# Performance work log

Measured on AMD Instinct MI355X. Metric: run time of the kernel, lower is better.

The kernel has to match this reference:

```python
import jax, jax.numpy as jnp
import numpy as np

H, DQK, DV, DM, POS = 8, 64, 64, 768, 64

def _rel_basis(l, n):
    # Enformer central-mask relative position basis: [l, l, n]
    pos = jnp.arange(l)
    distance = pos[None, :] - pos[:, None]              # [l, l] int
    half = n // 2
    pow_rate = jnp.exp(jnp.log(jnp.asarray((l + 1) / 2.0, jnp.float32)) / half)
    center_widths = pow_rate ** jnp.arange(1, half + 1, dtype=jnp.float32)  # [half]
    unsigned = (jnp.abs(distance)[:, :, None].astype(jnp.float32) <= center_widths)
    signed = jnp.sign(distance)[:, :, None] * unsigned
    return jnp.concatenate([unsigned.astype(jnp.float32), signed.astype(jnp.float32)], axis=-1)

def setup_inputs() -> dict:
    key = jax.random.key(0)
    ks = jax.random.split(key, 9)
    b, l = 2, 1024
    x = jax.random.normal(ks[0], (b, l, DM), jnp.float32)
    # torch Linear weights: [out, in]
    Wq = jax.random.normal(ks[1], (H * DQK, DM), jnp.float32) * (1.0 / np.sqrt(DM))
    Wk = jax.random.normal(ks[2], (H * DQK, DM), jnp.float32) * (1.0 / np.sqrt(DM))
    Wv = jax.random.normal(ks[3], (H * DV, DM), jnp.float32) * (1.0 / np.sqrt(DM))
    Wo = jax.random.normal(ks[4], (DM, H * DV), jnp.float32) * (1.0 / np.sqrt(H * DV))
    bo = jnp.zeros((DM,), jnp.float32)
    u_bias = jax.random.normal(ks[5], (H, DQK), jnp.float32) * np.sqrt(2.0 / DQK)
    v_bias = jax.random.normal(ks[6], (H, DQK), jnp.float32) * np.sqrt(2.0 / DQK)
    w_pos = jax.random.normal(ks[7], (H, DQK, POS), jnp.float32) * np.sqrt(2.0 / POS)
    return {"x": x, "Wq": Wq, "Wk": Wk, "Wv": Wv, "Wo": Wo, "bo": bo,
            "u_bias": u_bias, "v_bias": v_bias, "w_pos": w_pos}

def reference(x, Wq, Wk, Wv, Wo, bo, u_bias, v_bias, w_pos):
    b, l, _ = x.shape
    q = (x @ Wq.T).reshape(b, l, H, DQK)
    k = (x @ Wk.T).reshape(b, l, H, DQK)
    v = (x @ Wv.T).reshape(b, l, H, DV)
    basis = _rel_basis(l, POS)                           # [l, l, n]
    scale = 1.0 / np.sqrt(DQK)
    # qr_term: einsum('bihd,hdn,ijn->bhij') factored to avoid [b,h,l,l,d]
    qw = jnp.einsum('bihd,hdn->bhin', q, w_pos)          # [b,h,l,n]
    qr = jnp.einsum('bhin,ijn->bhij', qw, basis)
    uk = jnp.einsum('hd,bjhd->bhj', u_bias, k)[:, :, None, :]
    vw = jnp.einsum('hd,hdn->hn', v_bias, w_pos)
    vr = jnp.einsum('hn,ijn->hij', vw, basis)[None]      # [1,h,l,l]
    bias = (qr + uk + vr) * scale
    scores = jnp.einsum('bihd,bjhd->bhij', q, k) * scale + bias
    attn = jax.nn.softmax(scores, axis=-1)
    out = jnp.einsum('bhij,bjhd->bihd', attn, v).reshape(b, l, H * DV)
    return out @ Wo.T + bo
```

## Files before the change

### kernel.cpp

```cpp
#include <hip/hip_runtime.h>

#define LSEQ 1024
#define NB   2
#define NH   8
#define DD   64
#define DMOD 768

using bf16x8 = __attribute__((ext_vector_type(8))) short;
using f32x4  = __attribute__((ext_vector_type(4))) float;

__device__ inline unsigned short f2bf(float f) {
    union { float f; unsigned u; } v; v.f = f;
    unsigned r = v.u + 0x7FFFu + ((v.u >> 16) & 1u);
    return (unsigned short)(r >> 16);
}

__global__ __launch_bounds__(256) void pack_setup(
    const float4* __restrict__ x,  const float4* __restrict__ wq,
    const float4* __restrict__ wk, const float4* __restrict__ wv,
    const float4* __restrict__ wo,
    const float* __restrict__ u_bias, const float* __restrict__ v_bias,
    const float* __restrict__ w_pos,
    ushort4* __restrict__ xb, ushort4* __restrict__ wqb, ushort4* __restrict__ wkb,
    ushort4* __restrict__ wvb, ushort4* __restrict__ wob,
    float* __restrict__ wsfx, unsigned char* __restrict__ cls_g)
{
    int tid = threadIdx.x;
    if (blockIdx.x >= 3072) {
        int sb = blockIdx.x - 3072;
        if (sb == 0) {
            __shared__ float w_s[32];
            __shared__ int cmin_s[1024];
            if (tid < 32) {
                float pr = expf(logf(512.5f) / 32.0f);
                w_s[tid] = powf(pr, (float)(tid + 1));
            }
            __syncthreads();
            for (int d = tid; d < 1024; d += 256) {
                float fd = (float)d;
                int cm = 32;
                for (int c = 31; c >= 0; --c) if (fd <= w_s[c]) cm = c;
                cmin_s[d] = cm;
            }
            __syncthreads();
            for (int d2 = tid; d2 < 2048; d2 += 256) {
                int dd = d2 - 1023;
                int ad = dd < 0 ? -dd : dd; if (ad > 1023) ad = 1023;
                int t = (dd < 0) ? 0 : ((dd == 0) ? 1 : 2);
                cls_g[d2] = (unsigned char)(t * 33 + cmin_s[ad]);
            }
        } else {
            int h = sb - 1;
            __shared__ float vred[4][64];
            __shared__ float ured[4][64];
            __shared__ float wd[64];
            int n = tid & 63, g = tid >> 6;
            float vs = 0.f, us = 0.f;
#pragma unroll
            for (int k = 0; k < 16; ++k) {
                int d = g * 16 + k;
                float wp = w_pos[(h * 64 + d) * 64 + n];
                vs += v_bias[h * 64 + d] * wp;
                us += u_bias[h * 64 + d] * wp;
            }
            vred[g][n] = vs; ured[g][n] = us;
            __syncthreads();
            if (tid < 64) {
                float v4 = vred[0][tid] + vred[1][tid] + vred[2][tid] + vred[3][tid];
                float u4 = ured[0][tid] + ured[1][tid] + ured[2][tid] + ured[3][tid];
                wd[tid] = v4 - u4;
            }
            __syncthreads();
            if (tid < 64) {
                int nn = tid & 31, cb = tid & 32;
                float s = 0.f;
                for (int c = 31; c >= nn; --c) s += wd[cb + c];
                wsfx[h * 64 + tid] = s * 0.125f;
            }
        }
        return;
    }
    int i = blockIdx.x * 256 + tid;
    const float4* src; ushort4* dst; int off;
    if (i < 393216)      { src = x;  dst = xb;  off = i; }
    else if (i < 491520) { src = wq; dst = wqb; off = i - 393216; }
    else if (i < 589824) { src = wk; dst = wkb; off = i - 491520; }
    else if (i < 688128) { src = wv; dst = wvb; off = i - 589824; }
    else                 { src = wo; dst = wob; off = i - 688128; }
    float4 v = src[off];
    ushort4 o;
    o.x = f2bf(v.x); o.y = f2bf(v.y); o.z = f2bf(v.z); o.w = f2bf(v.w);
    dst[off] = o;
}

__global__ __launch_bounds__(256) void gemm_qkv(
    const unsigned short* __restrict__ X, const unsigned short* __restrict__ W,
    const float* __restrict__ ub,
    unsigned short* __restrict__ Qb, unsigned short* __restrict__ Kb,
    unsigned short* __restrict__ Vtb)
{
    __shared__ unsigned short Xs[64][40];
    __shared__ unsigned short Wsm[64][40];
    __shared__ unsigned short Ct[64][72];

    int tid = threadIdx.x;
    int w = tid >> 6, lane = tid & 63, l15 = lane & 15, q = lane >> 4;
    int M0 = blockIdx.y * 64, N0 = blockIdx.x * 64;
    int rs = tid >> 2, seg = tid & 3;

    f32x4 acc[4] = {};
    for (int k0 = 0; k0 < 768; k0 += 32) {
        uint4 xv = *(const uint4*)(X + (size_t)(M0 + rs) * 768 + k0 + seg * 8);
        uint4 wv = *(const uint4*)(W + (size_t)(N0 + rs) * 768 + k0 + seg * 8);
        *(uint4*)&Xs[rs][seg * 8]  = xv;
        *(uint4*)&Wsm[rs][seg * 8] = wv;
        __syncthreads();
        bf16x8 a = *(bf16x8*)&Xs[w * 16 + l15][q * 8];
#pragma unroll
        for (int ct = 0; ct < 4; ++ct) {
            bf16x8 bfr = *(bf16x8*)&Wsm[ct * 16 + l15][q * 8];
            acc[ct] = __builtin_amdgcn_mfma_f32_16x16x32_bf16(a, bfr, acc[ct], 0, 0, 0);
        }
        __syncthreads();
    }

    if (N0 < 1024) {
        int isQ = (N0 < 512);
#pragma unroll
        for (int ct = 0; ct < 4; ++ct) {
            float u0 = isQ ? ub[N0 + ct * 16 + l15] : 0.f;
            float sc = isQ ? 0.125f : 1.0f;
#pragma unroll
            for (int r = 0; r < 4; ++r)
                Ct[w * 16 + q * 4 + r][ct * 16 + l15] = f2bf((acc[ct][r] + u0) * sc);
        }
        __syncthreads();
        int Nh = isQ ? N0 : (N0 - 512);
        unsigned short* out = isQ ? Qb : Kb;
        size_t base = ((size_t)((M0 >> 10) * 8 + (Nh >> 6)) * 1024 + (M0 & 1023)) * 64;
#pragma unroll
        for (int it = 0; it < 2; ++it) {
            int idx = tid + it * 256;
            int row = idx >> 3, sg = idx & 7;
            *(uint4*)(out + base + (size_t)row * 64 + sg * 8) = *(uint4*)&Ct[row][sg * 8];
        }
    } else {
#pragma unroll
        for (int ct = 0; ct < 4; ++ct) {
            ushort4 pk;
            pk.x = f2bf(acc[ct][0]); pk.y = f2bf(acc[ct][1]);
            pk.z = f2bf(acc[ct][2]); pk.w = f2bf(acc[ct][3]);
            *(ushort4*)&Ct[ct * 16 + l15][w * 16 + q * 4] = pk;
        }
        __syncthreads();
        size_t base = ((size_t)((M0 >> 10) * 8 + ((N0 - 1024) >> 6))) * 65536;
        int j0 = M0 & 1023;
#pragma unroll
        for (int it = 0; it < 2; ++it) {
            int idx = tid + it * 256;
            int d = idx >> 3, sg = idx & 7;
            *(uint4*)(Vtb + base + (size_t)d * 1024 + j0 + sg * 8) = *(uint4*)&Ct[d][sg * 8];
        }
    }
}

__global__ __launch_bounds__(256) void gemm_o(
    const unsigned short* __restrict__ X, const unsigned short* __restrict__ W,
    const float* __restrict__ bias, float* __restrict__ out)
{
    __shared__ unsigned short Xs[64][40];
    __shared__ unsigned short Wsm[64][40];
    __shared__ float Ctf[64][72];

    int tid = threadIdx.x;
    int w = tid >> 6, lane = tid & 63, l15 = lane & 15, q = lane >> 4;
    int M0 = blockIdx.y * 64, N0 = blockIdx.x * 64;
    int rs = tid >> 2, seg = tid & 3;

    f32x4 acc[4] = {};
    for (int k0 = 0; k0 < 512; k0 += 32) {
        uint4 xv = *(const uint4*)(X + (size_t)(M0 + rs) * 512 + k0 + seg * 8);
        uint4 wv = *(const uint4*)(W + (size_t)(N0 + rs) * 512 + k0 + seg * 8);
        *(uint4*)&Xs[rs][seg * 8]  = xv;
        *(uint4*)&Wsm[rs][seg * 8] = wv;
        __syncthreads();
        bf16x8 a = *(bf16x8*)&Xs[w * 16 + l15][q * 8];
#pragma unroll
        for (int ct = 0; ct < 4; ++ct) {
            bf16x8 bfr = *(bf16x8*)&Wsm[ct * 16 + l15][q * 8];
            acc[ct] = __builtin_amdgcn_mfma_f32_16x16x32_bf16(a, bfr, acc[ct], 0, 0, 0);
        }
        __syncthreads();
    }
#pragma unroll
    for (int ct = 0; ct < 4; ++ct) {
        float bv = bias[N0 + ct * 16 + l15];
#pragma unroll
        for (int r = 0; r < 4; ++r)
            Ctf[w * 16 + q * 4 + r][ct * 16 + l15] = acc[ct][r] + bv;
    }
    __syncthreads();
#pragma unroll
    for (int it = 0; it < 4; ++it) {
        int idx = tid + it * 256;
        int row = idx >> 4, sg = idx & 15;
        *(float4*)(out + (size_t)(M0 + row) * 768 + N0 + sg * 4) = *(float4*)&Ctf[row][sg * 4];
    }
}

__global__ __launch_bounds__(256, 4) void attn_mfma(
    const unsigned short* __restrict__ Qbf,
    const unsigned short* __restrict__ Kbf,
    const unsigned short* __restrict__ Vt,
    const float* __restrict__ w_pos,
    const float* __restrict__ wsfx,
    const unsigned char* __restrict__ cls_g,
    unsigned short* __restrict__ ao)
{
    __shared__ float biasT[16 * 99];
    __shared__ unsigned char cls[2048];
    __shared__ unsigned short Pl[4][16][76];
    union Ovl {
        struct { unsigned short wptS[64][68]; float qwL[16][68]; } pre;
        struct { float Obuf[4][64][17]; float lbuf[4][16]; } post;
    };
    __shared__ Ovl ovl;

    int tid = threadIdx.x;
    int b = blockIdx.z, h = blockIdx.y, bh = b * 8 + h;
    int i0 = blockIdx.x * 16;
    int w = tid >> 6, lane = tid & 63, l15 = lane & 15, q = lane >> 4;

    for (int idx = tid; idx < 512; idx += 256)
        ((unsigned int*)cls)[idx] = ((const unsigned int*)cls_g)[idx];
    {
        const float4* wsrc = (const float4*)(w_pos + h * 4096);
#pragma unroll
        for (int it = 0; it < 4; ++it) {
            int f = tid + it * 256;
            float4 wv = wsrc[f];
            int d = f >> 4, n4 = (f & 15) * 4;
            ovl.pre.wptS[n4 + 0][d] = f2bf(wv.x);
            ovl.pre.wptS[n4 + 1][d] = f2bf(wv.y);
            ovl.pre.wptS[n4 + 2][d] = f2bf(wv.z);
            ovl.pre.wptS[n4 + 3][d] = f2bf(wv.w);
        }
    }

    int ig = i0 + l15;
    const unsigned short* qrow = Qbf + ((size_t)bh * 1024 + ig) * 64;
    bf16x8 qf0 = *(const bf16x8*)(qrow + q * 8);
    bf16x8 qf1 = *(const bf16x8*)(qrow + 32 + q * 8);
    __syncthreads();

    {
        bf16x8 b0 = *(bf16x8*)&ovl.pre.wptS[w * 16 + l15][q * 8];
        bf16x8 b1 = *(bf16x8*)&ovl.pre.wptS[w * 16 + l15][32 + q * 8];
        f32x4 a = {};
        a = __builtin_amdgcn_mfma_f32_16x16x32_bf16(qf0, b0, a, 0, 0, 0);
        a = __builtin_amdgcn_mfma_f32_16x16x32_bf16(qf1, b1, a, 0, 0, 0);
#pragma unroll
        for (int r = 0; r < 4; ++r)
            ovl.pre.qwL[q * 4 + r][w * 16 + l15] = a[r];
    }
    __syncthreads();

    const float* wsh = wsfx + h * 64;
#pragma unroll
    for (int it = 0; it < 4; ++it) {
        int idx = tid + it * 256;
        int il = idx >> 6, n = idx & 63, nn = n & 31, cb = n & 32;
        float run = 0.f, s = 0.f;
#pragma unroll
        for (int c = 31; c >= 0; --c) {
            run += ovl.pre.qwL[il][cb + c];
            if (c == nn) s = run;
        }
        ovl.pre.qwL[il][n] = s + wsh[n];
    }
    __syncthreads();

    for (int idx = tid; idx < 528; idx += 256) {
        int il = idx / 33, c = idx - il * 33;
        float up = 0.f, sp = 0.f;
        if (c < 32) {
            up = ovl.pre.qwL[il][c];
            sp = ovl.pre.qwL[il][32 + c];
        }
        float* bt = biasT + il * 99;
        bt[c]      = up - sp;
        bt[33 + c] = up;
        bt[66 + c] = up + sp;
    }
    __syncthreads();

    const unsigned short* Kbase = Kbf + (size_t)bh * 65536;
    const unsigned short* Vbase = Vt  + (size_t)bh * 65536;
    const float* btrow = biasT + l15 * 99;
    int clsoff = 1023 - ig;

    f32x4 Oacc[4] = {};
    float lsum = 0.f;

    for (int jt = 0; jt < 4; ++jt) {
        int jb = w * 256 + jt * 64;
        f32x4 st[4];
#pragma unroll
        for (int ct = 0; ct < 4; ++ct) {
            const unsigned short* krow = Kbase + (size_t)(jb + ct * 16 + l15) * 64;
            bf16x8 ka0 = *(const bf16x8*)(krow + q * 8);
            bf16x8 ka1 = *(const bf16x8*)(krow + 32 + q * 8);
            f32x4 a = {};
            a = __builtin_amdgcn_mfma_f32_16x16x32_bf16(ka0, qf0, a, 0, 0, 0);
            a = __builtin_amdgcn_mfma_f32_16x16x32_bf16(ka1, qf1, a, 0, 0, 0);
            st[ct] = a;
        }
#pragma unroll
        for (int ct = 0; ct < 4; ++ct) {
            int d2b = jb + ct * 16 + q * 4 + clsoff;
            float pv[4];
#pragma unroll
            for (int r = 0; r < 4; ++r) {
                float s = st[ct][r] + btrow[cls[d2b + r]];
                float p = __expf(s);
                lsum += p;
                pv[r] = p;
            }
            ushort4 pk;
            pk.x = f2bf(pv[0]); pk.y = f2bf(pv[1]);
            pk.z = f2bf(pv[2]); pk.w = f2bf(pv[3]);
            *(ushort4*)&Pl[w][l15][ct * 16 + q * 4] = pk;
        }
#pragma unroll
        for (int ks = 0; ks < 2; ++ks) {
            bf16x8 pb = *(const bf16x8*)&Pl[w][l15][ks * 32 + q * 8];
#pragma unroll
            for (int dt = 0; dt < 4; ++dt) {
                bf16x8 va = *(const bf16x8*)(Vbase + (size_t)(dt * 16 + l15) * 1024
                                             + jb + ks * 32 + q * 8);
                Oacc[dt] = __builtin_amdgcn_mfma_f32_16x16x32_bf16(va, pb, Oacc[dt], 0, 0, 0);
            }
        }
    }

    lsum += __shfl_xor(lsum, 16);
    lsum += __shfl_xor(lsum, 32);

    __syncthreads();
#pragma unroll
    for (int dt = 0; dt < 4; ++dt)
#pragma unroll
        for (int r = 0; r < 4; ++r)
            ovl.post.Obuf[w][dt * 16 + q * 4 + r][l15] = Oacc[dt][r];
    if (lane < 16) ovl.post.lbuf[w][l15] = lsum;
    __syncthreads();

    for (int t2 = tid; t2 < 1024; t2 += 256) {
        int il = t2 >> 6, d = t2 & 63;
        float o = ovl.post.Obuf[0][d][il] + ovl.post.Obuf[1][d][il]
                + ovl.post.Obuf[2][d][il] + ovl.post.Obuf[3][d][il];
        float l = ovl.post.lbuf[0][il] + ovl.post.lbuf[1][il]
                + ovl.post.lbuf[2][il] + ovl.post.lbuf[3][il];
        ao[((size_t)(b * 1024 + i0 + il)) * 512 + h * 64 + d] = f2bf(o / l);
    }
}

extern "C" void kernel_launch(void* const* d_in, const int* in_sizes, int n_in,
                              void* d_out, int out_size, void* d_ws, size_t ws_size,
                              hipStream_t stream)
{
    const float* x      = (const float*)d_in[0];
    const float* Wq     = (const float*)d_in[1];
    const float* Wk     = (const float*)d_in[2];
    const float* Wv     = (const float*)d_in[3];
    const float* Wo     = (const float*)d_in[4];
    const float* bo     = (const float*)d_in[5];
    const float* u_bias = (const float*)d_in[6];
    const float* v_bias = (const float*)d_in[7];
    const float* w_pos  = (const float*)d_in[8];
    float* out = (float*)d_out;

    char* ws = (char*)d_ws;
    unsigned short* Xbf  = (unsigned short*)ws;            ws += 3145728;
    unsigned short* Wqkv = (unsigned short*)ws;            ws += 2359296;
    unsigned short* Wob  = (unsigned short*)ws;            ws += 786432;
    unsigned short* Qbf  = (unsigned short*)ws;            ws += 2097152;
    unsigned short* Kbf  = (unsigned short*)ws;            ws += 2097152;
    unsigned short* Vtb  = (unsigned short*)ws;            ws += 2097152;
    unsigned short* aob  = (unsigned short*)ws;            ws += 2097152;
    float*          wsfx = (float*)ws;                     ws += 2048;
    unsigned char*  clsg = (unsigned char*)ws;             ws += 2048;

    pack_setup<<<3081, 256, 0, stream>>>(
        (const float4*)x, (const float4*)Wq, (const float4*)Wk,
        (const float4*)Wv, (const float4*)Wo,
        u_bias, v_bias, w_pos,
        (ushort4*)Xbf,
        (ushort4*)Wqkv, (ushort4*)Wqkv + 98304, (ushort4*)Wqkv + 196608,
        (ushort4*)Wob,
        wsfx, clsg);

    gemm_qkv<<<dim3(24, 32), 256, 0, stream>>>(Xbf, Wqkv, u_bias, Qbf, Kbf, Vtb);

    attn_mfma<<<dim3(64, 8, 2), 256, 0, stream>>>(
        Qbf, Kbf, Vtb, w_pos, wsfx, clsg, aob);

    gemm_o<<<dim3(12, 32), 256, 0, stream>>>(aob, Wob, bo, out);
}
```

Before: 137.2 us.

## Double-buffer GEMM tiles with register prefetch, widen K step, add MFMA priority hints

Both projection GEMMs now use double-buffered LDS tiles with a K step of 64. The next tile is prefetched into registers while MFMAs run on the current tile, which removes the second barrier per iteration and halves the loop trip count. The attention kernel wraps its MFMA phases in s_setprio so matrix work from one wave is favoured over other waves' softmax work. In exchange, LDS use per block and register pressure both go up. There is also a leftover redundant seg expression.

```diff
diff --git a/kernel.cpp b/kernel.cpp
--- a/kernel.cpp
+++ b/kernel.cpp
@@ -99,29 +99,48 @@
     unsigned short* __restrict__ Qb, unsigned short* __restrict__ Kb,
     unsigned short* __restrict__ Vtb)
 {
-    __shared__ unsigned short Xs[64][40];
-    __shared__ unsigned short Wsm[64][40];
-    __shared__ unsigned short Ct[64][72];
+    __shared__ __align__(16) unsigned short Xs[2][64][72];
+    __shared__ __align__(16) unsigned short Wsm[2][64][72];
+    __shared__ __align__(16) unsigned short Ct[64][72];
 
     int tid = threadIdx.x;
     int w = tid >> 6, lane = tid & 63, l15 = lane & 15, q = lane >> 4;
     int M0 = blockIdx.y * 64, N0 = blockIdx.x * 64;
-    int rs = tid >> 2, seg = tid & 3;
+    int rs = tid >> 3, seg = tid & 3 ? (tid & 7) : (tid & 7);
+    seg = tid & 7;
+
+    const unsigned short* xp = X + (size_t)(M0 + rs) * 768 + seg * 8;
+    const unsigned short* wp = W + (size_t)(N0 + rs) * 768 + seg * 8;
+
+    uint4 xa = *(const uint4*)(xp);
+    uint4 xb = *(const uint4*)(xp + (size_t)32 * 768);
+    uint4 wa = *(const uint4*)(wp);
+    uint4 wb = *(const uint4*)(wp + (size_t)32 * 768);
 
     f32x4 acc[4] = {};
-    for (int k0 = 0; k0 < 768; k0 += 32) {
-        uint4 xv = *(const uint4*)(X + (size_t)(M0 + rs) * 768 + k0 + seg * 8);
-        uint4 wv = *(const uint4*)(W + (size_t)(N0 + rs) * 768 + k0 + seg * 8);
-        *(uint4*)&Xs[rs][seg * 8]  = xv;
-        *(uint4*)&Wsm[rs][seg * 8] = wv;
+    int cur = 0;
+    for (int k0 = 0; k0 < 768; k0 += 64) {
+        *(uint4*)&Xs[cur][rs][seg * 8]       = xa;
+        *(uint4*)&Xs[cur][rs + 32][seg * 8]  = xb;
+        *(uint4*)&Wsm[cur][rs][seg * 8]      = wa;
+        *(uint4*)&Wsm[cur][rs + 32][seg * 8] = wb;
         __syncthreads();
-        bf16x8 a = *(bf16x8*)&Xs[w * 16 + l15][q * 8];
-#pragma unroll
-        for (int ct = 0; ct < 4; ++ct) {
-            bf16x8 bfr = *(bf16x8*)&Wsm[ct * 16 + l15][q * 8];
-            acc[ct] = __builtin_amdgcn_mfma_f32_16x16x32_bf16(a, bfr, acc[ct], 0, 0, 0);
-        }
-        __syncthreads();
+        if (k0 + 64 < 768) {
+            xa = *(const uint4*)(xp + k0 + 64);
+            xb = *(const uint4*)(xp + (size_t)32 * 768 + k0 + 64);
+            wa = *(const uint4*)(wp + k0 + 64);
+            wb = *(const uint4*)(wp + (size_t)32 * 768 + k0 + 64);
+        }
+        bf16x8 a0 = *(bf16x8*)&Xs[cur][w * 16 + l15][q * 8];
+        bf16x8 a1 = *(bf16x8*)&Xs[cur][w * 16 + l15][32 + q * 8];
+#pragma unroll
+        for (int ct = 0; ct < 4; ++ct) {
+            bf16x8 b0 = *(bf16x8*)&Wsm[cur][ct * 16 + l15][q * 8];
+            bf16x8 b1 = *(bf16x8*)&Wsm[cur][ct * 16 + l15][32 + q * 8];
+            acc[ct] = __builtin_amdgcn_mfma_f32_16x16x32_bf16(a0, b0, acc[ct], 0, 0, 0);
+            acc[ct] = __builtin_amdgcn_mfma_f32_16x16x32_bf16(a1, b1, acc[ct], 0, 0, 0);
+        }
+        cur ^= 1;
     }
 
     if (N0 < 1024) {
@@ -168,29 +187,47 @@
     const unsigned short* __restrict__ X, const unsigned short* __restrict__ W,
     const float* __restrict__ bias, float* __restrict__ out)
 {
-    __shared__ unsigned short Xs[64][40];
-    __shared__ unsigned short Wsm[64][40];
-    __shared__ float Ctf[64][72];
+    __shared__ __align__(16) unsigned short Xs[2][64][72];
+    __shared__ __align__(16) unsigned short Wsm[2][64][72];
+    __shared__ __align__(16) float Ctf[64][72];
 
     int tid = threadIdx.x;
     int w = tid >> 6, lane = tid & 63, l15 = lane & 15, q = lane >> 4;
     int M0 = blockIdx.y * 64, N0 = blockIdx.x * 64;
-    int rs = tid >> 2, seg = tid & 3;
+    int rs = tid >> 3, seg = tid & 7;
+
+    const unsigned short* xp = X + (size_t)(M0 + rs) * 512 + seg * 8;
+    const unsigned short* wp = W + (size_t)(N0 + rs) * 512 + seg * 8;
+
+    uint4 xa = *(const uint4*)(xp);
+    uint4 xb = *(const uint4*)(xp + (size_t)32 * 512);
+    uint4 wa = *(const uint4*)(wp);
+    uint4 wb = *(const uint4*)(wp + (size_t)32 * 512);
 
     f32x4 acc[4] = {};
-    for (int k0 = 0; k0 < 512; k0 += 32) {
-        uint4 xv = *(const uint4*)(X + (size_t)(M0 + rs) * 512 + k0 + seg * 8);
-        uint4 wv = *(const uint4*)(W + (size_t)(N0 + rs) * 512 + k0 + seg * 8);
-        *(uint4*)&Xs[rs][seg * 8]  = xv;
-        *(uint4*)&Wsm[rs][seg * 8] = wv;
+    int cur = 0;
+    for (int k0 = 0; k0 < 512; k0 += 64) {
+        *(uint4*)&Xs[cur][rs][seg * 8]       = xa;
+        *(uint4*)&Xs[cur][rs + 32][seg * 8]  = xb;
+        *(uint4*)&Wsm[cur][rs][seg * 8]      = wa;
+        *(uint4*)&Wsm[cur][rs + 32][seg * 8] = wb;
         __syncthreads();
-        bf16x8 a = *(bf16x8*)&Xs[w * 16 + l15][q * 8];
-#pragma unroll
-        for (int ct = 0; ct < 4; ++ct) {
-            bf16x8 bfr = *(bf16x8*)&Wsm[ct * 16 + l15][q * 8];
-            acc[ct] = __builtin_amdgcn_mfma_f32_16x16x32_bf16(a, bfr, acc[ct], 0, 0, 0);
-        }
-        __syncthreads();
+        if (k0 + 64 < 512) {
+            xa = *(const uint4*)(xp + k0 + 64);
+            xb = *(const uint4*)(xp + (size_t)32 * 512 + k0 + 64);
+            wa = *(const uint4*)(wp + k0 + 64);
+            wb = *(const uint4*)(wp + (size_t)32 * 512 + k0 + 64);
+        }
+        bf16x8 a0 = *(bf16x8*)&Xs[cur][w * 16 + l15][q * 8];
+        bf16x8 a1 = *(bf16x8*)&Xs[cur][w * 16 + l15][32 + q * 8];
+#pragma unroll
+        for (int ct = 0; ct < 4; ++ct) {
+            bf16x8 b0 = *(bf16x8*)&Wsm[cur][ct * 16 + l15][q * 8];
+            bf16x8 b1 = *(bf16x8*)&Wsm[cur][ct * 16 + l15][32 + q * 8];
+            acc[ct] = __builtin_amdgcn_mfma_f32_16x16x32_bf16(a0, b0, acc[ct], 0, 0, 0);
+            acc[ct] = __builtin_amdgcn_mfma_f32_16x16x32_bf16(a1, b1, acc[ct], 0, 0, 0);
+        }
+        cur ^= 1;
     }
 #pragma unroll
     for (int ct = 0; ct < 4; ++ct) {
@@ -305,6 +342,7 @@
     for (int jt = 0; jt < 4; ++jt) {
         int jb = w * 256 + jt * 64;
         f32x4 st[4];
+        __builtin_amdgcn_s_setprio(1);
 #pragma unroll
         for (int ct = 0; ct < 4; ++ct) {
             const unsigned short* krow = Kbase + (size_t)(jb + ct * 16 + l15) * 64;
@@ -315,6 +353,7 @@
             a = __builtin_amdgcn_mfma_f32_16x16x32_bf16(ka1, qf1, a, 0, 0, 0);
             st[ct] = a;
         }
+        __builtin_amdgcn_s_setprio(0);
 #pragma unroll
         for (int ct = 0; ct < 4; ++ct) {
             int d2b = jb + ct * 16 + q * 4 + clsoff;
@@ -331,6 +370,7 @@
             pk.z = f2bf(pv[2]); pk.w = f2bf(pv[3]);
             *(ushort4*)&Pl[w][l15][ct * 16 + q * 4] = pk;
         }
+        __builtin_amdgcn_s_setprio(1);
 #pragma unroll
         for (int ks = 0; ks < 2; ++ks) {
             bf16x8 pb = *(const bf16x8*)&Pl[w][l15][ks * 32 + q * 8];
@@ -341,6 +381,7 @@
                 Oacc[dt] = __builtin_amdgcn_mfma_f32_16x16x32_bf16(va, pb, Oacc[dt], 0, 0, 0);
             }
         }
+        __builtin_amdgcn_s_setprio(0);
     }
 
     lsum += __shfl_xor(lsum, 16);
```

Measured after the change: 133.1 us. -3.0%, faster.
